# Performance work log

Measured on AMD Instinct MI355X. Metric: run time of the kernel, lower is better.

Reference implementation:

```python
import jax, jax.numpy as jnp
import numpy as np

BSZ, SEQ, DIM, NH = 2, 2048, 2048, 16
HD = DIM // NH  # 128


def setup_inputs() -> dict:
    key = jax.random.key(0)
    ks = jax.random.split(key, 6)
    x = jax.random.normal(ks[0], (BSZ, SEQ, DIM), dtype=jnp.float32)
    # torch Linear weights: [out_features, in_features]
    scale = 1.0 / np.sqrt(DIM)
    wq = jax.random.normal(ks[1], (DIM, DIM), dtype=jnp.float32) * scale
    wk = jax.random.normal(ks[2], (DIM, DIM), dtype=jnp.float32) * scale
    wv = jax.random.normal(ks[3], (DIM, DIM), dtype=jnp.float32) * scale
    wo = jax.random.normal(ks[4], (DIM, DIM), dtype=jnp.float32) * scale
    # RoPE freqs (llama style): theta=10000
    inv_freq = 1.0 / (10000.0 ** (jnp.arange(0, HD, 2, dtype=jnp.float32) / HD))  # [HD//2]
    t = jnp.arange(SEQ, dtype=jnp.float32)
    angles = jnp.outer(t, inv_freq)  # [SEQ, HD//2]
    freqs_cos = jnp.cos(angles)
    freqs_sin = jnp.sin(angles)
    # causal additive mask [SEQ, SEQ]
    mask = jnp.where(jnp.tril(jnp.ones((SEQ, SEQ), dtype=bool)), 0.0, -jnp.inf).astype(jnp.float32)
    return {"x": x, "wq": wq, "wk": wk, "wv": wv, "wo": wo,
            "freqs_cos": freqs_cos, "freqs_sin": freqs_sin, "mask": mask}


def _apply_rope(v, cos, sin):
    # v: [b, s, h, hd]; complex pairs are interleaved (even=real, odd=imag)
    b, s, h, hd = v.shape
    vr = v.reshape(b, s, h, hd // 2, 2)
    v0, v1 = vr[..., 0], vr[..., 1]
    c = cos[None, :, None, :]  # [1, s, 1, hd//2]
    sn = sin[None, :, None, :]
    out = jnp.stack([v0 * c - v1 * sn, v0 * sn + v1 * c], axis=-1)
    return out.reshape(b, s, h, hd)


def reference(x, wq, wk, wv, wo, freqs_cos, freqs_sin, mask):
    b, s, _ = x.shape
    xq = (x @ wq.T).reshape(b, s, NH, HD)
    xk = (x @ wk.T).reshape(b, s, NH, HD)
    xv = (x @ wv.T).reshape(b, s, NH, HD)
    xq = _apply_rope(xq, freqs_cos, freqs_sin)
    xk = _apply_rope(xk, freqs_cos, freqs_sin)
    # [b, h, s, s]
    scores = jnp.einsum('bqhd,bkhd->bhqk', xq, xk) / jnp.sqrt(jnp.float32(HD))
    scores = scores + mask[None, None, :, :]
    probs = jax.nn.softmax(scores.astype(jnp.float32), axis=-1).astype(scores.dtype)
    out = jnp.einsum('bhqk,bkhd->bqhd', probs, xv).reshape(b, s, NH * HD)
    return out @ wo.T
```

## Files before the change

### kernel.cpp

```cpp
#include <hip/hip_runtime.h>
#include <hip/hip_bf16.h>
#include <stdint.h>

typedef __bf16 bf16x8 __attribute__((ext_vector_type(8)));
typedef float f32x4 __attribute__((ext_vector_type(4)));
typedef unsigned short u16;
typedef unsigned int u32;

#define DEVI __device__ __forceinline__

DEVI u16 f2b(float f){ __bf16 h = (__bf16)f; return __builtin_bit_cast(u16, h); }
DEVI float b2f(u16 u){ return (float)__builtin_bit_cast(__bf16, u); }

constexpr int BSZ = 2, SEQ = 2048, DIM = 2048, NH = 16, HD = 128;

#if defined(__has_builtin)
#if __has_builtin(__builtin_amdgcn_global_load_lds)
#define HAVE_ASYNC_LDS 1
#endif
#endif

DEVI void cp16(void* lds, const void* g){
#ifdef HAVE_ASYNC_LDS
  auto gp = (const __attribute__((address_space(1))) u32*)(uintptr_t)g;
  auto lp = (__attribute__((address_space(3))) u32*)(uintptr_t)lds;
  __builtin_amdgcn_global_load_lds(gp, lp, 16, 0, 0);
#else
  *(uint4*)lds = *(const uint4*)g;
#endif
}

__global__ __launch_bounds__(256) void k_convert(
    const float* __restrict__ x, const float* __restrict__ wq,
    const float* __restrict__ wk, const float* __restrict__ wv,
    const float* __restrict__ wo,
    u16* __restrict__ xb, u16* __restrict__ wqkv, u16* __restrict__ wob)
{
  int e = (blockIdx.x * 256 + threadIdx.x) * 4;
  float4 v; u16* dp;
  if (e < 8388608){
    v = *(const float4*)&x[e]; dp = &xb[e];
  } else if (e < 20971520){
    int o = e - 8388608; int sec = o >> 22; int oo = o & 4194303;
    const float* w = (sec == 0) ? wq : ((sec == 1) ? wk : wv);
    v = *(const float4*)&w[oo]; dp = &wqkv[o];
  } else {
    int o = e - 20971520;
    v = *(const float4*)&wo[o]; dp = &wob[o];
  }
  ushort4 r; r.x = f2b(v.x); r.y = f2b(v.y); r.z = f2b(v.z); r.w = f2b(v.w);
  *(ushort4*)dp = r;
}

__global__ __launch_bounds__(256) void k_gemm_qkv(
    const u16* __restrict__ A, const u16* __restrict__ W,
    u16* __restrict__ Qd, u16* __restrict__ Kd, u16* __restrict__ Vd)
{
  __shared__ u16 As[128*32];
  __shared__ u16 Bs[128*32];
  const int t = threadIdx.x;
  const int lane = t & 63;
  const int l15 = lane & 15, quad = lane >> 4;
  const int wave = t >> 6;
  const int wr = (wave >> 1) * 64, wc = (wave & 1) * 64;
  const int tm = blockIdx.y * 128, tn = blockIdx.x * 128;
  const int arow = t >> 2, acol = (t & 3) * 8;

  f32x4 acc[4][4] = {};
  for (int k0 = 0; k0 < DIM; k0 += 32){
    __syncthreads();
    #pragma unroll
    for (int is = 0; is < 2; ++is){
      int row = is*64 + arow;
      cp16(&As[is*2048 + t*8], &A[(size_t)(tm + row)*DIM + k0 + acol]);
      cp16(&Bs[is*2048 + t*8], &W[(size_t)(tn + row)*DIM + k0 + acol]);
    }
    __syncthreads();
    bf16x8 af[4], bf[4];
    #pragma unroll
    for (int i = 0; i < 4; ++i){
      af[i] = *(const bf16x8*)&As[(wr + i*16 + l15)*32 + quad*8];
      bf[i] = *(const bf16x8*)&Bs[(wc + i*16 + l15)*32 + quad*8];
    }
    #pragma unroll
    for (int mt = 0; mt < 4; ++mt)
      #pragma unroll
      for (int nt = 0; nt < 4; ++nt)
        acc[mt][nt] = __builtin_amdgcn_mfma_f32_16x16x32_bf16(af[mt], bf[nt], acc[mt][nt], 0, 0, 0);
  }
  #pragma unroll
  for (int mt = 0; mt < 4; ++mt)
    #pragma unroll
    for (int nt = 0; nt < 4; ++nt)
      #pragma unroll
      for (int r = 0; r < 4; ++r){
        int row = tm + wr + mt*16 + quad*4 + r;
        int col = tn + wc + nt*16 + l15;
        int sec = col >> 11, nn = col & 2047;
        int h = nn >> 7, d = nn & 127;
        int b = row >> 11, s = row & 2047;
        u16* dst = (sec == 0) ? Qd : ((sec == 1) ? Kd : Vd);
        dst[(((size_t)(b*NH + h))*SEQ + s)*HD + d] = f2b(acc[mt][nt][r]);
      }
}

__global__ __launch_bounds__(256) void k_rope(
    u16* __restrict__ Qd, u16* __restrict__ Kd,
    const float* __restrict__ fc, const float* __restrict__ fs)
{
  int p = blockIdx.x * 256 + threadIdx.x;
  int isK = p >> 22;
  int pi = p & 4194303;
  int bh = pi >> 17;
  int rem = pi & 131071;
  int s = rem >> 6, i = rem & 63;
  u16* ptr = isK ? Kd : Qd;
  float scale = isK ? 1.0f : (0.08838834764831845f * 1.4426950408889634f);
  size_t base = ((size_t)bh*SEQ + s)*HD + 2*i;
  float v0 = b2f(ptr[base]), v1 = b2f(ptr[base + 1]);
  float c = fc[s*64 + i], sn = fs[s*64 + i];
  ptr[base]     = f2b((v0*c - v1*sn) * scale);
  ptr[base + 1] = f2b((v0*sn + v1*c) * scale);
}

__global__ __launch_bounds__(256) void k_vtrans(
    const u16* __restrict__ V, u16* __restrict__ Vt)
{
  __shared__ u16 ts[64*72];
  const int t = threadIdx.x;
  const int st = blockIdx.x, dt = blockIdx.y, bh = blockIdx.z;
  const size_t base  = (size_t)bh * SEQ * HD;
  const size_t baseT = (size_t)bh * HD * SEQ;
  #pragma unroll
  for (int i = 0; i < 2; ++i){
    int s = i*32 + (t>>3), c = t&7;
    *(uint4*)&ts[s*72 + c*8] = *(const uint4*)&V[base + (size_t)(st*64 + s)*HD + dt*64 + c*8];
  }
  __syncthreads();
  #pragma unroll
  for (int i = 0; i < 2; ++i){
    int d = i*32 + (t>>3), sc = t&7;
    u16 tmp[8];
    #pragma unroll
    for (int j = 0; j < 8; ++j) tmp[j] = ts[(sc*8 + j)*72 + d];
    *(uint4*)&Vt[baseT + (size_t)(dt*64 + d)*SEQ + st*64 + sc*8] = *(const uint4*)tmp;
  }
}

__global__ __launch_bounds__(256) void k_flash(
    const u16* __restrict__ Qd, const u16* __restrict__ Kd,
    const u16* __restrict__ Vt, u16* __restrict__ Od)
{
  __shared__ u16 Ks[64*144];
  __shared__ u16 Vs[128*72];
  __shared__ u16 Ps[4*32*72];

  const int t = threadIdx.x, lane = t & 63, wave = t >> 6;
  const int l15 = lane & 15, quad = lane >> 4;
  const int h = blockIdx.y, b = blockIdx.z, bh = b*NH + h;
  const size_t base  = (size_t)bh * SEQ * HD;
  const size_t baseT = (size_t)bh * HD * SEQ;
  u16* Psw = &Ps[wave*32*72];

  const int krow = t >> 4, kcol = (t & 15) * 8;
  const int vrow = t >> 3, vcol = (t & 7) * 8;

  for (int pass = 0; pass < 2; ++pass){
    const int qt = pass ? (15 - (int)blockIdx.x) : (int)blockIdx.x;
    const int qb = qt*128 + wave*32;
    const int nkt = 2*qt + 2;

    bf16x8 qf[2][4];
    #pragma unroll
    for (int mt = 0; mt < 2; ++mt)
      #pragma unroll
      for (int ks = 0; ks < 4; ++ks)
        qf[mt][ks] = *(const bf16x8*)&Qd[base + (size_t)(qb + mt*16 + l15)*HD + ks*32 + quad*8];

    f32x4 oacc[8][2] = {};
    float m_s[2] = {-1e30f, -1e30f}, l_s[2] = {0.f, 0.f};

    uint4 kreg[4], vreg[4];
    #pragma unroll
    for (int i = 0; i < 4; ++i){
      kreg[i] = *(const uint4*)&Kd[base + (size_t)(i*16 + krow)*HD + kcol];
      vreg[i] = *(const uint4*)&Vt[baseT + (size_t)(i*32 + vrow)*SEQ + vcol];
    }

    for (int kt = 0; kt < nkt; ++kt){
      __syncthreads();
      #pragma unroll
      for (int i = 0; i < 4; ++i){
        *(uint4*)&Ks[(i*16 + krow)*144 + kcol] = kreg[i];
        *(uint4*)&Vs[(i*32 + vrow)*72 + vcol] = vreg[i];
      }
      __syncthreads();
      if (kt + 1 < nkt){
        #pragma unroll
        for (int i = 0; i < 4; ++i){
          kreg[i] = *(const uint4*)&Kd[base + (size_t)((kt+1)*64 + i*16 + krow)*HD + kcol];
          vreg[i] = *(const uint4*)&Vt[baseT + (size_t)(i*32 + vrow)*SEQ + (kt+1)*64 + vcol];
        }
      }
      if (kt*64 <= qb + 31){
        f32x4 sacc[4][2] = {};
        #pragma unroll
        for (int ks = 0; ks < 4; ++ks){
          bf16x8 kf[4];
          #pragma unroll
          for (int nk = 0; nk < 4; ++nk)
            kf[nk] = *(const bf16x8*)&Ks[(nk*16 + l15)*144 + ks*32 + quad*8];
          #pragma unroll
          for (int nk = 0; nk < 4; ++nk)
            #pragma unroll
            for (int mt = 0; mt < 2; ++mt)
              sacc[nk][mt] = __builtin_amdgcn_mfma_f32_16x16x32_bf16(kf[nk], qf[mt][ks], sacc[nk][mt], 0, 0, 0);
        }
        #pragma unroll
        for (int nk = 0; nk < 4; ++nk)
          #pragma unroll
          for (int mt = 0; mt < 2; ++mt){
            int q = qb + mt*16 + l15;
            #pragma unroll
            for (int r = 0; r < 4; ++r){
              int key = kt*64 + nk*16 + quad*4 + r;
              if (key > q) sacc[nk][mt][r] = -1e30f;
            }
          }
        #pragma unroll
        for (int mt = 0; mt < 2; ++mt){
          float rm = -1e30f;
          #pragma unroll
          for (int nk = 0; nk < 4; ++nk)
            #pragma unroll
            for (int r = 0; r < 4; ++r) rm = fmaxf(rm, sacc[nk][mt][r]);
          rm = fmaxf(rm, __shfl_xor(rm, 16));
          rm = fmaxf(rm, __shfl_xor(rm, 32));
          float mnew = fmaxf(m_s[mt], rm);
          float alpha = exp2f(m_s[mt] - mnew);
          m_s[mt] = mnew;
          float rs = 0.f;
          #pragma unroll
          for (int nk = 0; nk < 4; ++nk){
            u16 pk[4];
            #pragma unroll
            for (int r = 0; r < 4; ++r){
              float p = exp2f(sacc[nk][mt][r] - mnew);
              rs += p;
              pk[r] = f2b(p);
            }
            *(uint2*)&Psw[(mt*16 + l15)*72 + nk*16 + quad*4] = *(const uint2*)pk;
          }
          rs += __shfl_xor(rs, 16);
          rs += __shfl_xor(rs, 32);
          l_s[mt] = l_s[mt]*alpha + rs;
          #pragma unroll
          for (int db = 0; db < 8; ++db)
            #pragma unroll
            for (int r = 0; r < 4; ++r) oacc[db][mt][r] *= alpha;
        }
        #pragma unroll
        for (int k2 = 0; k2 < 2; ++k2){
          bf16x8 pf[2];
          #pragma unroll
          for (int mt = 0; mt < 2; ++mt)
            pf[mt] = *(const bf16x8*)&Psw[(mt*16 + l15)*72 + k2*32 + quad*8];
          #pragma unroll
          for (int db = 0; db < 8; ++db){
            bf16x8 vf = *(const bf16x8*)&Vs[(db*16 + l15)*72 + k2*32 + quad*8];
            #pragma unroll
            for (int mt = 0; mt < 2; ++mt)
              oacc[db][mt] = __builtin_amdgcn_mfma_f32_16x16x32_bf16(vf, pf[mt], oacc[db][mt], 0, 0, 0);
          }
        }
      }
    }
    #pragma unroll
    for (int mt = 0; mt < 2; ++mt){
      float inv = 1.0f / l_s[mt];
      int s = qb + mt*16 + l15;
      #pragma unroll
      for (int db = 0; db < 8; ++db){
        u16 ok[4];
        #pragma unroll
        for (int r = 0; r < 4; ++r) ok[r] = f2b(oacc[db][mt][r] * inv);
        *(uint2*)&Od[(((size_t)(b*SEQ + s))*NH + h)*HD + db*16 + quad*4] = *(const uint2*)ok;
      }
    }
  }
}

__global__ __launch_bounds__(256) void k_gemm_out(
    const u16* __restrict__ A, const u16* __restrict__ W, float* __restrict__ out)
{
  __shared__ u16 As[128*32];
  __shared__ u16 Bs[128*32];
  const int t = threadIdx.x;
  const int lane = t & 63;
  const int l15 = lane & 15, quad = lane >> 4;
  const int wave = t >> 6;
  const int wr = (wave >> 1) * 64, wc = (wave & 1) * 64;
  const int tm = blockIdx.y * 128, tn = blockIdx.x * 128;
  const int arow = t >> 2, acol = (t & 3) * 8;

  f32x4 acc[4][4] = {};
  for (int k0 = 0; k0 < DIM; k0 += 32){
    __syncthreads();
    #pragma unroll
    for (int is = 0; is < 2; ++is){
      int row = is*64 + arow;
      cp16(&As[is*2048 + t*8], &A[(size_t)(tm + row)*DIM + k0 + acol]);
      cp16(&Bs[is*2048 + t*8], &W[(size_t)(tn + row)*DIM + k0 + acol]);
    }
    __syncthreads();
    bf16x8 af[4], bf[4];
    #pragma unroll
    for (int i = 0; i < 4; ++i){
      af[i] = *(const bf16x8*)&As[(wr + i*16 + l15)*32 + quad*8];
      bf[i] = *(const bf16x8*)&Bs[(wc + i*16 + l15)*32 + quad*8];
    }
    #pragma unroll
    for (int mt = 0; mt < 4; ++mt)
      #pragma unroll
      for (int nt = 0; nt < 4; ++nt)
        acc[mt][nt] = __builtin_amdgcn_mfma_f32_16x16x32_bf16(af[mt], bf[nt], acc[mt][nt], 0, 0, 0);
  }
  #pragma unroll
  for (int mt = 0; mt < 4; ++mt)
    #pragma unroll
    for (int nt = 0; nt < 4; ++nt)
      #pragma unroll
      for (int r = 0; r < 4; ++r){
        int row = tm + wr + mt*16 + quad*4 + r;
        int col = tn + wc + nt*16 + l15;
        out[(size_t)row*DIM + col] = acc[mt][nt][r];
      }
}

extern "C" void kernel_launch(void* const* d_in, const int* in_sizes, int n_in,
                              void* d_out, int out_size, void* d_ws, size_t ws_size,
                              hipStream_t stream)
{
  const float* x  = (const float*)d_in[0];
  const float* wq = (const float*)d_in[1];
  const float* wk = (const float*)d_in[2];
  const float* wv = (const float*)d_in[3];
  const float* wo = (const float*)d_in[4];
  const float* fc = (const float*)d_in[5];
  const float* fs = (const float*)d_in[6];
  float* out = (float*)d_out;

  char* ws = (char*)d_ws;
  u16* xb   = (u16*)(ws);
  u16* wqkv = (u16*)(ws + 16777216);
  u16* wob  = (u16*)(ws + 41943040);
  u16* Qr   = (u16*)(ws + 50331648);
  u16* Kr   = (u16*)(ws + 67108864);
  u16* Vr   = (u16*)(ws + 83886080);
  u16* Ob   = (u16*)(ws + 100663296);
  u16* VtT  = xb;

  k_convert <<<24576, 256, 0, stream>>>(x, wq, wk, wv, wo, xb, wqkv, wob);
  k_gemm_qkv<<<dim3(48, 32), 256, 0, stream>>>(xb, wqkv, Qr, Kr, Vr);
  k_rope    <<<32768, 256, 0, stream>>>(Qr, Kr, fc, fs);
  k_vtrans  <<<dim3(32, 2, 32), 256, 0, stream>>>(Vr, VtT);
  k_flash   <<<dim3(8, NH, BSZ), 256, 0, stream>>>(Qr, Kr, VtT, Ob);
  k_gemm_out<<<dim3(16, 32), 256, 0, stream>>>(Ob, wob, out);
}
```

Measured before the change: 470.5 us.

## Fuse RoPE into QKV GEMM epilogue and split flash attention KV range

Moves RoPE and the Q scaling into the QKV GEMM epilogue by staging the output tile through LDS, which drops the separate RoPE pass over Q/K and gives coalesced 16-byte stores. The flash kernel now splits each paired query-tile workload's combined KV range into two halves across twice as many blocks (512 instead of 256), so more CUs are busy. Each split writes unnormalized partial outputs plus running max and sum, and a new combine kernel merges them. This adds extra bf16 partial-output traffic, a combine launch, and reuse of workspace buffers for the partials.

```diff
diff --git a/kernel.cpp b/kernel.cpp
--- a/kernel.cpp
+++ b/kernel.cpp
@@ -54,7 +54,291 @@
 
 __global__ __launch_bounds__(256) void k_gemm_qkv(
     const u16* __restrict__ A, const u16* __restrict__ W,
+    const float* __restrict__ fc, const float* __restrict__ fs,
     u16* __restrict__ Qd, u16* __restrict__ Kd, u16* __restrict__ Vd)
+{
+  __shared__ u16 As[128*32];
+  __shared__ u16 Bs[128*32];
+  __shared__ u16 Cs[128*136];
+  const int t = threadIdx.x;
+  const int lane = t & 63;
+  const int l15 = lane & 15, quad = lane >> 4;
+  const int wave = t >> 6;
+  const int wr = (wave >> 1) * 64, wc = (wave & 1) * 64;
+  const int tm = blockIdx.y * 128, tn = blockIdx.x * 128;
+  const int arow = t >> 2, acol = (t & 3) * 8;
+
+  f32x4 acc[4][4] = {};
+  for (int k0 = 0; k0 < DIM; k0 += 32){
+    __syncthreads();
+    #pragma unroll
+    for (int is = 0; is < 2; ++is){
+      int row = is*64 + arow;
+      cp16(&As[is*2048 + t*8], &A[(size_t)(tm + row)*DIM + k0 + acol]);
+      cp16(&Bs[is*2048 + t*8], &W[(size_t)(tn + row)*DIM + k0 + acol]);
+    }
+    __syncthreads();
+    bf16x8 af[4], bfr[4];
+    #pragma unroll
+    for (int i = 0; i < 4; ++i){
+      af[i]  = *(const bf16x8*)&As[(wr + i*16 + l15)*32 + quad*8];
+      bfr[i] = *(const bf16x8*)&Bs[(wc + i*16 + l15)*32 + quad*8];
+    }
+    #pragma unroll
+    for (int mt = 0; mt < 4; ++mt)
+      #pragma unroll
+      for (int nt = 0; nt < 4; ++nt)
+        acc[mt][nt] = __builtin_amdgcn_mfma_f32_16x16x32_bf16(af[mt], bfr[nt], acc[mt][nt], 0, 0, 0);
+  }
+  #pragma unroll
+  for (int mt = 0; mt < 4; ++mt)
+    #pragma unroll
+    for (int nt = 0; nt < 4; ++nt)
+      #pragma unroll
+      for (int r = 0; r < 4; ++r)
+        Cs[(wr + mt*16 + quad*4 + r)*136 + wc + nt*16 + l15] = f2b(acc[mt][nt][r]);
+  __syncthreads();
+
+  const int sec = tn >> 11;
+  const int hh = (tn & 2047) >> 7;
+  u16* dst = (sec == 0) ? Qd : ((sec == 1) ? Kd : Vd);
+  const float qs = (sec == 0) ? (0.08838834764831845f * 1.4426950408889634f) : 1.0f;
+  const int col0 = (t & 15) * 8;
+  #pragma unroll
+  for (int jj = 0; jj < 8; ++jj){
+    int row = (t >> 4) + jj*16;
+    int m = tm + row;
+    int b = m >> 11, s = m & 2047;
+    uint4 cv = *(const uint4*)&Cs[row*136 + col0];
+    const u16* cp = (const u16*)&cv;
+    u16 op[8];
+    if (sec < 2){
+      float4 c4 = *(const float4*)&fc[(size_t)s*64 + (col0 >> 1)];
+      float4 s4 = *(const float4*)&fs[(size_t)s*64 + (col0 >> 1)];
+      float cc[4] = {c4.x*qs, c4.y*qs, c4.z*qs, c4.w*qs};
+      float ss[4] = {s4.x*qs, s4.y*qs, s4.z*qs, s4.w*qs};
+      #pragma unroll
+      for (int p = 0; p < 4; ++p){
+        float a = b2f(cp[2*p]), bb = b2f(cp[2*p+1]);
+        op[2*p]   = f2b(a*cc[p] - bb*ss[p]);
+        op[2*p+1] = f2b(a*ss[p] + bb*cc[p]);
+      }
+    } else {
+      #pragma unroll
+      for (int p = 0; p < 8; ++p) op[p] = cp[p];
+    }
+    *(uint4*)&dst[((size_t)(b*NH + hh)*SEQ + s)*HD + col0] = *(const uint4*)op;
+  }
+}
+
+__global__ __launch_bounds__(256) void k_vtrans(
+    const u16* __restrict__ V, u16* __restrict__ Vt)
+{
+  __shared__ u16 ts[64*72];
+  const int t = threadIdx.x;
+  const int st = blockIdx.x, dt = blockIdx.y, bh = blockIdx.z;
+  const size_t base  = (size_t)bh * SEQ * HD;
+  const size_t baseT = (size_t)bh * HD * SEQ;
+  #pragma unroll
+  for (int i = 0; i < 2; ++i){
+    int s = i*32 + (t>>3), c = t&7;
+    *(uint4*)&ts[s*72 + c*8] = *(const uint4*)&V[base + (size_t)(st*64 + s)*HD + dt*64 + c*8];
+  }
+  __syncthreads();
+  #pragma unroll
+  for (int i = 0; i < 2; ++i){
+    int d = i*32 + (t>>3), sc = t&7;
+    u16 tmp[8];
+    #pragma unroll
+    for (int j = 0; j < 8; ++j) tmp[j] = ts[(sc*8 + j)*72 + d];
+    *(uint4*)&Vt[baseT + (size_t)(dt*64 + d)*SEQ + st*64 + sc*8] = *(const uint4*)tmp;
+  }
+}
+
+__global__ __launch_bounds__(256) void k_flash(
+    const u16* __restrict__ Qd, const u16* __restrict__ Kd,
+    const u16* __restrict__ Vt, u16* __restrict__ OP0, u16* __restrict__ OP1,
+    float* __restrict__ Mp, float* __restrict__ Lp)
+{
+  __shared__ u16 Ks[64*144];
+  __shared__ u16 Vs[128*72];
+  __shared__ u16 Ps[4*32*72];
+
+  const int t = threadIdx.x, lane = t & 63, wave = t >> 6;
+  const int l15 = lane & 15, quad = lane >> 4;
+  const int j = blockIdx.x >> 1, split = blockIdx.x & 1;
+  const int h = blockIdx.y, b = blockIdx.z, bh = b*NH + h;
+  const size_t base  = (size_t)bh * SEQ * HD;
+  const size_t baseT = (size_t)bh * HD * SEQ;
+  u16* Psw = &Ps[wave*32*72];
+  u16* OPs = split ? OP1 : OP0;
+  const int lo = 17*split, hi = lo + 17;
+  const int qt0 = j, qt1 = 15 - j;
+  const int len0 = 2*qt0 + 2;
+
+  const int krow = t >> 4, kcol = (t & 15) * 8;
+  const int vrow = t >> 3, vcol = (t & 7) * 8;
+
+  for (int pass = 0; pass < 2; ++pass){
+    const int qt = pass ? qt1 : qt0;
+    const int len = 2*qt + 2;
+    int kt0 = pass ? (lo - len0) : lo; if (kt0 < 0) kt0 = 0;
+    int kt1 = pass ? (hi - len0) : hi; if (kt1 > len) kt1 = len;
+    const int qb = qt*128 + wave*32;
+
+    bf16x8 qf[2][4];
+    #pragma unroll
+    for (int mt = 0; mt < 2; ++mt)
+      #pragma unroll
+      for (int ks = 0; ks < 4; ++ks)
+        qf[mt][ks] = *(const bf16x8*)&Qd[base + (size_t)(qb + mt*16 + l15)*HD + ks*32 + quad*8];
+
+    f32x4 oacc[8][2] = {};
+    float m_s[2] = {-1e30f, -1e30f}, l_s[2] = {0.f, 0.f};
+
+    if (kt0 < kt1){
+      uint4 kreg[4], vreg[4];
+      #pragma unroll
+      for (int i = 0; i < 4; ++i){
+        kreg[i] = *(const uint4*)&Kd[base + (size_t)(kt0*64 + i*16 + krow)*HD + kcol];
+        vreg[i] = *(const uint4*)&Vt[baseT + (size_t)(i*32 + vrow)*SEQ + kt0*64 + vcol];
+      }
+      for (int kt = kt0; kt < kt1; ++kt){
+        __syncthreads();
+        #pragma unroll
+        for (int i = 0; i < 4; ++i){
+          *(uint4*)&Ks[(i*16 + krow)*144 + kcol] = kreg[i];
+          *(uint4*)&Vs[(i*32 + vrow)*72 + vcol] = vreg[i];
+        }
+        __syncthreads();
+        if (kt + 1 < kt1){
+          #pragma unroll
+          for (int i = 0; i < 4; ++i){
+            kreg[i] = *(const uint4*)&Kd[base + (size_t)((kt+1)*64 + i*16 + krow)*HD + kcol];
+            vreg[i] = *(const uint4*)&Vt[baseT + (size_t)(i*32 + vrow)*SEQ + (kt+1)*64 + vcol];
+          }
+        }
+        if (kt*64 <= qb + 31){
+          f32x4 sacc[4][2] = {};
+          #pragma unroll
+          for (int ks = 0; ks < 4; ++ks){
+            bf16x8 kf[4];
+            #pragma unroll
+            for (int nk = 0; nk < 4; ++nk)
+              kf[nk] = *(const bf16x8*)&Ks[(nk*16 + l15)*144 + ks*32 + quad*8];
+            #pragma unroll
+            for (int nk = 0; nk < 4; ++nk)
+              #pragma unroll
+              for (int mt = 0; mt < 2; ++mt)
+                sacc[nk][mt] = __builtin_amdgcn_mfma_f32_16x16x32_bf16(kf[nk], qf[mt][ks], sacc[nk][mt], 0, 0, 0);
+          }
+          #pragma unroll
+          for (int nk = 0; nk < 4; ++nk)
+            #pragma unroll
+            for (int mt = 0; mt < 2; ++mt){
+              int q = qb + mt*16 + l15;
+              #pragma unroll
+              for (int r = 0; r < 4; ++r){
+                int key = kt*64 + nk*16 + quad*4 + r;
+                if (key > q) sacc[nk][mt][r] = -1e30f;
+              }
+            }
+          #pragma unroll
+          for (int mt = 0; mt < 2; ++mt){
+            float rm = -1e30f;
+            #pragma unroll
+            for (int nk = 0; nk < 4; ++nk)
+              #pragma unroll
+              for (int r = 0; r < 4; ++r) rm = fmaxf(rm, sacc[nk][mt][r]);
+            rm = fmaxf(rm, __shfl_xor(rm, 16));
+            rm = fmaxf(rm, __shfl_xor(rm, 32));
+            float mnew = fmaxf(m_s[mt], rm);
+            float alpha = exp2f(m_s[mt] - mnew);
+            m_s[mt] = mnew;
+            float rs = 0.f;
+            #pragma unroll
+            for (int nk = 0; nk < 4; ++nk){
+              u16 pk[4];
+              #pragma unroll
+              for (int r = 0; r < 4; ++r){
+                float p = exp2f(sacc[nk][mt][r] - mnew);
+                rs += p;
+                pk[r] = f2b(p);
+              }
+              *(uint2*)&Psw[(mt*16 + l15)*72 + nk*16 + quad*4] = *(const uint2*)pk;
+            }
+            rs += __shfl_xor(rs, 16);
+            rs += __shfl_xor(rs, 32);
+            l_s[mt] = l_s[mt]*alpha + rs;
+            #pragma unroll
+            for (int db = 0; db < 8; ++db)
+              #pragma unroll
+              for (int r = 0; r < 4; ++r) oacc[db][mt][r] *= alpha;
+          }
+          #pragma unroll
+          for (int k2 = 0; k2 < 2; ++k2){
+            bf16x8 pf[2];
+            #pragma unroll
+            for (int mt = 0; mt < 2; ++mt)
+              pf[mt] = *(const bf16x8*)&Psw[(mt*16 + l15)*72 + k2*32 + quad*8];
+            #pragma unroll
+            for (int db = 0; db < 8; ++db){
+              bf16x8 vf = *(const bf16x8*)&Vs[(db*16 + l15)*72 + k2*32 + quad*8];
+              #pragma unroll
+              for (int mt = 0; mt < 2; ++mt)
+                oacc[db][mt] = __builtin_amdgcn_mfma_f32_16x16x32_bf16(vf, pf[mt], oacc[db][mt], 0, 0, 0);
+            }
+          }
+        }
+      }
+    }
+    #pragma unroll
+    for (int mt = 0; mt < 2; ++mt){
+      int s = qb + mt*16 + l15;
+      #pragma unroll
+      for (int db = 0; db < 8; ++db){
+        u16 ok[4];
+        #pragma unroll
+        for (int r = 0; r < 4; ++r) ok[r] = f2b(oacc[db][mt][r]);
+        *(uint2*)&OPs[(((size_t)(b*SEQ + s))*NH + h)*HD + db*16 + quad*4] = *(const uint2*)ok;
+      }
+      if (quad == 0){
+        size_t mi = ((size_t)split*BSZ*NH + bh)*SEQ + s;
+        Mp[mi] = m_s[mt];
+        Lp[mi] = l_s[mt];
+      }
+    }
+  }
+}
+
+__global__ __launch_bounds__(256) void k_combine(
+    u16* __restrict__ OP0, const u16* __restrict__ OP1,
+    const float* __restrict__ Mp, const float* __restrict__ Lp)
+{
+  size_t flat = ((size_t)blockIdx.x*256 + threadIdx.x)*8;
+  int h = (int)((flat >> 7) & 15);
+  int s = (int)((flat >> 11) & 2047);
+  int b = (int)(flat >> 22);
+  size_t row = ((size_t)(b*NH + h))*SEQ + s;
+  const size_t off1 = (size_t)BSZ*NH*SEQ;
+  float m0 = Mp[row], l0 = Lp[row];
+  float m1 = Mp[row + off1], l1 = Lp[row + off1];
+  float m = fmaxf(m0, m1);
+  float w0 = exp2f(m0 - m), w1 = exp2f(m1 - m);
+  float inv = 1.0f / (w0*l0 + w1*l1);
+  uint4 a = *(const uint4*)&OP0[flat];
+  uint4 c = *(const uint4*)&OP1[flat];
+  const u16* pa = (const u16*)&a;
+  const u16* pc = (const u16*)&c;
+  u16 o[8];
+  #pragma unroll
+  for (int i = 0; i < 8; ++i)
+    o[i] = f2b((b2f(pa[i])*w0 + b2f(pc[i])*w1) * inv);
+  *(uint4*)&OP0[flat] = *(const uint4*)o;
+}
+
+__global__ __launch_bounds__(256) void k_gemm_out(
+    const u16* __restrict__ A, const u16* __restrict__ W, float* __restrict__ out)
 {
   __shared__ u16 As[128*32];
   __shared__ u16 Bs[128*32];
@@ -76,254 +360,17 @@
       cp16(&Bs[is*2048 + t*8], &W[(size_t)(tn + row)*DIM + k0 + acol]);
     }
     __syncthreads();
-    bf16x8 af[4], bf[4];
+    bf16x8 af[4], bfr[4];
     #pragma unroll
     for (int i = 0; i < 4; ++i){
-      af[i] = *(const bf16x8*)&As[(wr + i*16 + l15)*32 + quad*8];
-      bf[i] = *(const bf16x8*)&Bs[(wc + i*16 + l15)*32 + quad*8];
+      af[i]  = *(const bf16x8*)&As[(wr + i*16 + l15)*32 + quad*8];
+      bfr[i] = *(const bf16x8*)&Bs[(wc + i*16 + l15)*32 + quad*8];
     }
     #pragma unroll
     for (int mt = 0; mt < 4; ++mt)
       #pragma unroll
       for (int nt = 0; nt < 4; ++nt)
-        acc[mt][nt] = __builtin_amdgcn_mfma_f32_16x16x32_bf16(af[mt], bf[nt], acc[mt][nt], 0, 0, 0);
-  }
-  #pragma unroll
-  for (int mt = 0; mt < 4; ++mt)
-    #pragma unroll
-    for (int nt = 0; nt < 4; ++nt)
-      #pragma unroll
-      for (int r = 0; r < 4; ++r){
-        int row = tm + wr + mt*16 + quad*4 + r;
-        int col = tn + wc + nt*16 + l15;
-        int sec = col >> 11, nn = col & 2047;
-        int h = nn >> 7, d = nn & 127;
-        int b = row >> 11, s = row & 2047;
-        u16* dst = (sec == 0) ? Qd : ((sec == 1) ? Kd : Vd);
-        dst[(((size_t)(b*NH + h))*SEQ + s)*HD + d] = f2b(acc[mt][nt][r]);
-      }
-}
-
-__global__ __launch_bounds__(256) void k_rope(
-    u16* __restrict__ Qd, u16* __restrict__ Kd,
-    const float* __restrict__ fc, const float* __restrict__ fs)
-{
-  int p = blockIdx.x * 256 + threadIdx.x;
-  int isK = p >> 22;
-  int pi = p & 4194303;
-  int bh = pi >> 17;
-  int rem = pi & 131071;
-  int s = rem >> 6, i = rem & 63;
-  u16* ptr = isK ? Kd : Qd;
-  float scale = isK ? 1.0f : (0.08838834764831845f * 1.4426950408889634f);
-  size_t base = ((size_t)bh*SEQ + s)*HD + 2*i;
-  float v0 = b2f(ptr[base]), v1 = b2f(ptr[base + 1]);
-  float c = fc[s*64 + i], sn = fs[s*64 + i];
-  ptr[base]     = f2b((v0*c - v1*sn) * scale);
-  ptr[base + 1] = f2b((v0*sn + v1*c) * scale);
-}
-
-__global__ __launch_bounds__(256) void k_vtrans(
-    const u16* __restrict__ V, u16* __restrict__ Vt)
-{
-  __shared__ u16 ts[64*72];
-  const int t = threadIdx.x;
-  const int st = blockIdx.x, dt = blockIdx.y, bh = blockIdx.z;
-  const size_t base  = (size_t)bh * SEQ * HD;
-  const size_t baseT = (size_t)bh * HD * SEQ;
-  #pragma unroll
-  for (int i = 0; i < 2; ++i){
-    int s = i*32 + (t>>3), c = t&7;
-    *(uint4*)&ts[s*72 + c*8] = *(const uint4*)&V[base + (size_t)(st*64 + s)*HD + dt*64 + c*8];
-  }
-  __syncthreads();
-  #pragma unroll
-  for (int i = 0; i < 2; ++i){
-    int d = i*32 + (t>>3), sc = t&7;
-    u16 tmp[8];
-    #pragma unroll
-    for (int j = 0; j < 8; ++j) tmp[j] = ts[(sc*8 + j)*72 + d];
-    *(uint4*)&Vt[baseT + (size_t)(dt*64 + d)*SEQ + st*64 + sc*8] = *(const uint4*)tmp;
-  }
-}
-
-__global__ __launch_bounds__(256) void k_flash(
-    const u16* __restrict__ Qd, const u16* __restrict__ Kd,
-    const u16* __restrict__ Vt, u16* __restrict__ Od)
-{
-  __shared__ u16 Ks[64*144];
-  __shared__ u16 Vs[128*72];
-  __shared__ u16 Ps[4*32*72];
-
-  const int t = threadIdx.x, lane = t & 63, wave = t >> 6;
-  const int l15 = lane & 15, quad = lane >> 4;
-  const int h = blockIdx.y, b = blockIdx.z, bh = b*NH + h;
-  const size_t base  = (size_t)bh * SEQ * HD;
-  const size_t baseT = (size_t)bh * HD * SEQ;
-  u16* Psw = &Ps[wave*32*72];
-
-  const int krow = t >> 4, kcol = (t & 15) * 8;
-  const int vrow = t >> 3, vcol = (t & 7) * 8;
-
-  for (int pass = 0; pass < 2; ++pass){
-    const int qt = pass ? (15 - (int)blockIdx.x) : (int)blockIdx.x;
-    const int qb = qt*128 + wave*32;
-    const int nkt = 2*qt + 2;
-
-    bf16x8 qf[2][4];
-    #pragma unroll
-    for (int mt = 0; mt < 2; ++mt)
-      #pragma unroll
-      for (int ks = 0; ks < 4; ++ks)
-        qf[mt][ks] = *(const bf16x8*)&Qd[base + (size_t)(qb + mt*16 + l15)*HD + ks*32 + quad*8];
-
-    f32x4 oacc[8][2] = {};
-    float m_s[2] = {-1e30f, -1e30f}, l_s[2] = {0.f, 0.f};
-
-    uint4 kreg[4], vreg[4];
-    #pragma unroll
-    for (int i = 0; i < 4; ++i){
-      kreg[i] = *(const uint4*)&Kd[base + (size_t)(i*16 + krow)*HD + kcol];
-      vreg[i] = *(const uint4*)&Vt[baseT + (size_t)(i*32 + vrow)*SEQ + vcol];
-    }
-
-    for (int kt = 0; kt < nkt; ++kt){
-      __syncthreads();
-      #pragma unroll
-      for (int i = 0; i < 4; ++i){
-        *(uint4*)&Ks[(i*16 + krow)*144 + kcol] = kreg[i];
-        *(uint4*)&Vs[(i*32 + vrow)*72 + vcol] = vreg[i];
-      }
-      __syncthreads();
-      if (kt + 1 < nkt){
-        #pragma unroll
-        for (int i = 0; i < 4; ++i){
-          kreg[i] = *(const uint4*)&Kd[base + (size_t)((kt+1)*64 + i*16 + krow)*HD + kcol];
-          vreg[i] = *(const uint4*)&Vt[baseT + (size_t)(i*32 + vrow)*SEQ + (kt+1)*64 + vcol];
-        }
-      }
-      if (kt*64 <= qb + 31){
-        f32x4 sacc[4][2] = {};
-        #pragma unroll
-        for (int ks = 0; ks < 4; ++ks){
-          bf16x8 kf[4];
-          #pragma unroll
-          for (int nk = 0; nk < 4; ++nk)
-            kf[nk] = *(const bf16x8*)&Ks[(nk*16 + l15)*144 + ks*32 + quad*8];
-          #pragma unroll
-          for (int nk = 0; nk < 4; ++nk)
-            #pragma unroll
-            for (int mt = 0; mt < 2; ++mt)
-              sacc[nk][mt] = __builtin_amdgcn_mfma_f32_16x16x32_bf16(kf[nk], qf[mt][ks], sacc[nk][mt], 0, 0, 0);
-        }
-        #pragma unroll
-        for (int nk = 0; nk < 4; ++nk)
-          #pragma unroll
-          for (int mt = 0; mt < 2; ++mt){
-            int q = qb + mt*16 + l15;
-            #pragma unroll
-            for (int r = 0; r < 4; ++r){
-              int key = kt*64 + nk*16 + quad*4 + r;
-              if (key > q) sacc[nk][mt][r] = -1e30f;
-            }
-          }
-        #pragma unroll
-        for (int mt = 0; mt < 2; ++mt){
-          float rm = -1e30f;
-          #pragma unroll
-          for (int nk = 0; nk < 4; ++nk)
-            #pragma unroll
-            for (int r = 0; r < 4; ++r) rm = fmaxf(rm, sacc[nk][mt][r]);
-          rm = fmaxf(rm, __shfl_xor(rm, 16));
-          rm = fmaxf(rm, __shfl_xor(rm, 32));
-          float mnew = fmaxf(m_s[mt], rm);
-          float alpha = exp2f(m_s[mt] - mnew);
-          m_s[mt] = mnew;
-          float rs = 0.f;
-          #pragma unroll
-          for (int nk = 0; nk < 4; ++nk){
-            u16 pk[4];
-            #pragma unroll
-            for (int r = 0; r < 4; ++r){
-              float p = exp2f(sacc[nk][mt][r] - mnew);
-              rs += p;
-              pk[r] = f2b(p);
-            }
-            *(uint2*)&Psw[(mt*16 + l15)*72 + nk*16 + quad*4] = *(const uint2*)pk;
-          }
-          rs += __shfl_xor(rs, 16);
-          rs += __shfl_xor(rs, 32);
-          l_s[mt] = l_s[mt]*alpha + rs;
-          #pragma unroll
-          for (int db = 0; db < 8; ++db)
-            #pragma unroll
-            for (int r = 0; r < 4; ++r) oacc[db][mt][r] *= alpha;
-        }
-        #pragma unroll
-        for (int k2 = 0; k2 < 2; ++k2){
-          bf16x8 pf[2];
-          #pragma unroll
-          for (int mt = 0; mt < 2; ++mt)
-            pf[mt] = *(const bf16x8*)&Psw[(mt*16 + l15)*72 + k2*32 + quad*8];
-          #pragma unroll
-          for (int db = 0; db < 8; ++db){
-            bf16x8 vf = *(const bf16x8*)&Vs[(db*16 + l15)*72 + k2*32 + quad*8];
-            #pragma unroll
-            for (int mt = 0; mt < 2; ++mt)
-              oacc[db][mt] = __builtin_amdgcn_mfma_f32_16x16x32_bf16(vf, pf[mt], oacc[db][mt], 0, 0, 0);
-          }
-        }
-      }
-    }
-    #pragma unroll
-    for (int mt = 0; mt < 2; ++mt){
-      float inv = 1.0f / l_s[mt];
-      int s = qb + mt*16 + l15;
-      #pragma unroll
-      for (int db = 0; db < 8; ++db){
-        u16 ok[4];
-        #pragma unroll
-        for (int r = 0; r < 4; ++r) ok[r] = f2b(oacc[db][mt][r] * inv);
-        *(uint2*)&Od[(((size_t)(b*SEQ + s))*NH + h)*HD + db*16 + quad*4] = *(const uint2*)ok;
-      }
-    }
-  }
-}
-
-__global__ __launch_bounds__(256) void k_gemm_out(
-    const u16* __restrict__ A, const u16* __restrict__ W, float* __restrict__ out)
-{
-  __shared__ u16 As[128*32];
-  __shared__ u16 Bs[128*32];
-  const int t = threadIdx.x;
-  const int lane = t & 63;
-  const int l15 = lane & 15, quad = lane >> 4;
-  const int wave = t >> 6;
-  const int wr = (wave >> 1) * 64, wc = (wave & 1) * 64;
-  const int tm = blockIdx.y * 128, tn = blockIdx.x * 128;
-  const int arow = t >> 2, acol = (t & 3) * 8;
-
-  f32x4 acc[4][4] = {};
-  for (int k0 = 0; k0 < DIM; k0 += 32){
-    __syncthreads();
-    #pragma unroll
-    for (int is = 0; is < 2; ++is){
-      int row = is*64 + arow;
-      cp16(&As[is*2048 + t*8], &A[(size_t)(tm + row)*DIM + k0 + acol]);
-      cp16(&Bs[is*2048 + t*8], &W[(size_t)(tn + row)*DIM + k0 + acol]);
-    }
-    __syncthreads();
-    bf16x8 af[4], bf[4];
-    #pragma unroll
-    for (int i = 0; i < 4; ++i){
-      af[i] = *(const bf16x8*)&As[(wr + i*16 + l15)*32 + quad*8];
-      bf[i] = *(const bf16x8*)&Bs[(wc + i*16 + l15)*32 + quad*8];
-    }
-    #pragma unroll
-    for (int mt = 0; mt < 4; ++mt)
-      #pragma unroll
-      for (int nt = 0; nt < 4; ++nt)
-        acc[mt][nt] = __builtin_amdgcn_mfma_f32_16x16x32_bf16(af[mt], bf[nt], acc[mt][nt], 0, 0, 0);
+        acc[mt][nt] = __builtin_amdgcn_mfma_f32_16x16x32_bf16(af[mt], bfr[nt], acc[mt][nt], 0, 0, 0);
   }
   #pragma unroll
   for (int mt = 0; mt < 4; ++mt)
@@ -359,11 +406,14 @@
   u16* Vr   = (u16*)(ws + 83886080);
   u16* Ob   = (u16*)(ws + 100663296);
   u16* VtT  = xb;
+  u16* OP1  = wqkv;
+  float* Mp = (float*)(ws + 33554432);
+  float* Lp = (float*)(ws + 34078720);
 
   k_convert <<<24576, 256, 0, stream>>>(x, wq, wk, wv, wo, xb, wqkv, wob);
-  k_gemm_qkv<<<dim3(48, 32), 256, 0, stream>>>(xb, wqkv, Qr, Kr, Vr);
-  k_rope    <<<32768, 256, 0, stream>>>(Qr, Kr, fc, fs);
+  k_gemm_qkv<<<dim3(48, 32), 256, 0, stream>>>(xb, wqkv, fc, fs, Qr, Kr, Vr);
   k_vtrans  <<<dim3(32, 2, 32), 256, 0, stream>>>(Vr, VtT);
-  k_flash   <<<dim3(8, NH, BSZ), 256, 0, stream>>>(Qr, Kr, VtT, Ob);
+  k_flash   <<<dim3(16, NH, BSZ), 256, 0, stream>>>(Qr, Kr, VtT, Ob, OP1, Mp, Lp);
+  k_combine <<<4096, 256, 0, stream>>>(Ob, OP1, Mp, Lp);
   k_gemm_out<<<dim3(16, 32), 256, 0, stream>>>(Ob, wob, out);
 }
```

Result: slower. 489.3 us (+4.0%).
